# Kernel optimization log

Measured on AMD Instinct MI355X. Metric: run time of the kernel, lower is better.

## Reference

```python
import jax, jax.numpy as jnp
import numpy as np
import math

B, N, E, D = 8, 2048, 2048, 128
MAX_K = 8
HYPER_DIM = 128
LN_EPS = 1e-5


def _sinusoidal_pe(max_pos, dim):
    pe = np.zeros((max_pos, dim), dtype=np.float32)
    position = np.arange(max_pos, dtype=np.float32)[:, None]
    div_term = np.exp(np.arange(0, dim, 2, dtype=np.float32) * (-math.log(10000.0) / dim))
    pe[:, 0::2] = np.sin(position * div_term)
    pe[:, 1::2] = np.cos(position * div_term)
    return jnp.asarray(pe)


def setup_inputs() -> dict:
    key = jax.random.key(0)
    ks = jax.random.split(key, 24)
    s = 0.05
    inp = {
        'x_v': jax.random.normal(ks[0], (B, N, D), jnp.float32),
        'x_e': jax.random.normal(ks[1], (B, E, D), jnp.float32),
        'incidence': (jax.random.uniform(ks[2], (B, N, E), jnp.float32) < 0.01).astype(jnp.float32),
        'suffix_normalizer': jax.random.uniform(ks[3], (B, N), jnp.float32) * 20.0,
        'edge_orders': 1 + jax.random.randint(ks[4], (B, E), 0, MAX_K),
        'node_mask': jax.random.randint(ks[5], (B, N), 0, 2) > 0,
        'edge_mask': jax.random.randint(ks[6], (B, E), 0, 2) > 0,
        'pe1_table': _sinusoidal_pe(MAX_K + 1, D),
        'pe2_table': _sinusoidal_pe(2, D),
        'bias_b': jax.random.uniform(ks[7], (1, D), jnp.float32, -1, 1) / math.sqrt(D),
    }
    i = 8
    for m in ('mlp1', 'mlp2', 'mlp3'):
        inp[m + '_W1'] = jax.random.normal(ks[i], (D, HYPER_DIM), jnp.float32) * s; i += 1
        inp[m + '_b1'] = jnp.zeros((HYPER_DIM,), jnp.float32)
        inp[m + '_W2'] = jax.random.normal(ks[i], (HYPER_DIM, D), jnp.float32) * s; i += 1
        inp[m + '_b2'] = jnp.zeros((D,), jnp.float32)
    for n in ('norm1', 'norm2', 'norm3'):
        inp[n + '_g'] = jnp.ones((D,), jnp.float32)
        inp[n + '_b'] = jnp.zeros((D,), jnp.float32)
    return inp


def _ln(x, g, b):
    mu = jnp.mean(x, axis=-1, keepdims=True)
    var = jnp.mean(jnp.square(x - mu), axis=-1, keepdims=True)
    return (x - mu) * jax.lax.rsqrt(var + LN_EPS) * g + b


def _mlp(x, W1, b1, W2, b2):
    return jax.nn.relu(x @ W1 + b1) @ W2 + b2


def reference(x_v, x_e, incidence, suffix_normalizer, edge_orders, node_mask, edge_mask,
              pe1_table, pe2_table, bias_b,
              mlp1_W1, mlp1_b1, mlp1_W2, mlp1_b2,
              mlp2_W1, mlp2_b1, mlp2_W2, mlp2_b2,
              mlp3_W1, mlp3_b1, mlp3_W2, mlp3_b2,
              norm1_g, norm1_b, norm2_g, norm2_b, norm3_g, norm3_b):
    nm = node_mask[..., None]  # [B,N,1]
    em = edge_mask[..., None]  # [B,E,1]
    x_v = jnp.where(nm, x_v, 0.0)
    x_e = jnp.where(em, x_e, 0.0)
    pe1_k1 = pe1_table[1][None, None, :]          # [1,1,D]
    pe1_k = pe1_table[edge_orders]                # [B,E,D]
    x_v = x_v + _mlp(_ln(x_v, norm1_g, norm1_b) + pe1_k1, mlp1_W1, mlp1_b1, mlp1_W2, mlp1_b2)
    x_e = x_e + _mlp(_ln(x_e, norm1_g, norm1_b) + pe1_k, mlp1_W1, mlp1_b1, mlp1_W2, mlp1_b2)
    x_v = jnp.where(nm, x_v, 0.0)
    x_e = jnp.where(em, x_e, 0.0)
    agg = jnp.einsum('bne,bed->bnd', incidence, x_e)
    x1 = x_v + agg / (1.0 + suffix_normalizer[..., None])
    pe2_s1 = pe2_table[1][None, None, :]
    x1 = x1 + _mlp(_ln(x1, norm2_g, norm2_b) + pe2_s1, mlp2_W1, mlp2_b1, mlp2_W2, mlp2_b2)
    x = jnp.where(nm, x1, 0.0)
    x = x + _mlp(_ln(x, norm3_g, norm3_b), mlp3_W1, mlp3_b1, mlp3_W2, mlp3_b2)
    x = x + bias_b
    x = jnp.where(nm, x, 0.0)
    return x
```

## Files before the change

kernel.cpp:

```cpp
#include <hip/hip_runtime.h>
#include <stdint.h>

#define BB 8
#define NN 2048
#define EE 2048
#define DD 128
#define RBP 132
#define NTHREADS 256
#define WMAT_U32 8192
#define SCANB 2048
#define LCAP 64

typedef __attribute__((ext_vector_type(8))) short bf16x8;
typedef __attribute__((ext_vector_type(4))) float f32x4;

__device__ inline unsigned bf16rne(float f) {
    unsigned u = __float_as_uint(f);
    return (u + 0x7fffu + ((u >> 16) & 1u)) >> 16;
}
__device__ inline float bf16lo(unsigned u) { return __uint_as_float(u << 16); }
__device__ inline float bf16hi(unsigned u) { return __uint_as_float(u & 0xffff0000u); }

#define SWZ(b) ((b) ^ ((((b) >> 8) & 7) << 4))

struct __align__(16) SmemK1 {
    float rowbuf[32][RBP];
    unsigned h[32 * DD / 2];
    int rmask[32];
    int ords[32];
};

struct __align__(16) SmemK2 {
    float rowbuf[16][RBP];
    unsigned h[16 * DD / 2];
    int rmask[16];
};

__device__ inline void load_rows32(SmemK1& s, const float* __restrict__ src) {
    int t = threadIdx.x;
    for (int idx = t; idx < 32 * 32; idx += NTHREADS) {
        int r = idx >> 5, c4 = (idx & 31) * 4;
        float4 v = *(const float4*)&src[r * DD + c4];
        *(float4*)&s.rowbuf[r][c4] = v;
    }
    __syncthreads();
}

__device__ inline void ln32(SmemK1& s, const float* __restrict__ gw,
                            const float* __restrict__ bw,
                            const float* __restrict__ pe_base, bool per_row_pe) {
    int t = threadIdx.x;
    int gr = t >> 3, g = t & 7;
    int base = g * 16;
    float x[16];
    float4* xp = (float4*)x;
    xp[0] = *(const float4*)&s.rowbuf[gr][base + 0];
    xp[1] = *(const float4*)&s.rowbuf[gr][base + 4];
    xp[2] = *(const float4*)&s.rowbuf[gr][base + 8];
    xp[3] = *(const float4*)&s.rowbuf[gr][base + 12];
    float s1 = 0.f, s2 = 0.f;
    #pragma unroll
    for (int i = 0; i < 16; i++) { s1 += x[i]; s2 += x[i] * x[i]; }
    #pragma unroll
    for (int off = 1; off < 8; off <<= 1) {
        s1 += __shfl_xor(s1, off, 64);
        s2 += __shfl_xor(s2, off, 64);
    }
    float mu = s1 * (1.f / 128.f);
    float var = s2 * (1.f / 128.f) - mu * mu;
    float rstd = rsqrtf(var + 1e-5f);
    const float* pe = nullptr;
    if (pe_base) pe = per_row_pe ? (pe_base + (size_t)s.ords[gr] * DD) : pe_base;
    unsigned p[8];
    #pragma unroll
    for (int j = 0; j < 8; j++) {
        int k0 = base + 2 * j;
        float v0 = (x[2 * j] - mu) * rstd * gw[k0] + bw[k0];
        float v1 = (x[2 * j + 1] - mu) * rstd * gw[k0 + 1] + bw[k0 + 1];
        if (pe) { v0 += pe[k0]; v1 += pe[k0 + 1]; }
        p[j] = bf16rne(v0) | (bf16rne(v1) << 16);
    }
    char* hb = (char*)s.h;
    int byte0 = gr * 256 + g * 32;
    uint4 lo = make_uint4(p[0], p[1], p[2], p[3]);
    uint4 hi = make_uint4(p[4], p[5], p[6], p[7]);
    *(uint4*)(hb + SWZ(byte0)) = lo;
    *(uint4*)(hb + SWZ(byte0 + 16)) = hi;
    __syncthreads();
}

template <bool TO_H>
__device__ inline void mm32_f32w(SmemK1& s, const float* __restrict__ Wf,
                                 const float* __restrict__ bias) {
    int t = threadIdx.x;
    int w = t >> 6, l = t & 63;
    int lm = l & 15, lk = l >> 4;
    bf16x8 bfr[2][4];
    #pragma unroll
    for (int nbl = 0; nbl < 2; nbl++) {
        int n = w * 32 + nbl * 16 + lm;
        #pragma unroll
        for (int kb = 0; kb < 4; kb++) {
            int k0 = kb * 32 + lk * 8;
            unsigned pk[4];
            #pragma unroll
            for (int jp = 0; jp < 4; jp++) {
                float a = Wf[(size_t)(k0 + 2 * jp) * DD + n];
                float b = Wf[(size_t)(k0 + 2 * jp + 1) * DD + n];
                pk[jp] = bf16rne(a) | (bf16rne(b) << 16);
            }
            uint4 u = make_uint4(pk[0], pk[1], pk[2], pk[3]);
            bfr[nbl][kb] = *(bf16x8*)&u;
        }
    }
    const char* hb = (const char*)s.h;
    bf16x8 afr[2][4];
    #pragma unroll
    for (int mb = 0; mb < 2; mb++) {
        int row = mb * 16 + lm;
        #pragma unroll
        for (int kb = 0; kb < 4; kb++)
            afr[mb][kb] = *(const bf16x8*)(hb + SWZ(row * 256 + kb * 64 + lk * 16));
    }
    f32x4 acc[2][2];
    #pragma unroll
    for (int mb = 0; mb < 2; mb++)
        #pragma unroll
        for (int nbl = 0; nbl < 2; nbl++)
            acc[mb][nbl] = (f32x4){0.f, 0.f, 0.f, 0.f};
    #pragma unroll
    for (int kb = 0; kb < 4; kb++)
        #pragma unroll
        for (int mb = 0; mb < 2; mb++)
            #pragma unroll
            for (int nbl = 0; nbl < 2; nbl++)
                acc[mb][nbl] = __builtin_amdgcn_mfma_f32_16x16x32_bf16(
                    afr[mb][kb], bfr[nbl][kb], acc[mb][nbl], 0, 0, 0);
    float bcol0 = bias[w * 32 + lm];
    float bcol1 = bias[w * 32 + 16 + lm];
    __syncthreads();
    if (TO_H) {
        char* hw = (char*)s.h;
        #pragma unroll
        for (int mb = 0; mb < 2; mb++)
            #pragma unroll
            for (int nbl = 0; nbl < 2; nbl++) {
                int col = w * 32 + nbl * 16 + lm;
                float bc = nbl ? bcol1 : bcol0;
                #pragma unroll
                for (int j = 0; j < 4; j++) {
                    int row = mb * 16 + lk * 4 + j;
                    float v = fmaxf(acc[mb][nbl][j] + bc, 0.f);
                    *(unsigned short*)(hw + SWZ(row * 256 + col * 2)) =
                        (unsigned short)bf16rne(v);
                }
            }
    } else {
        #pragma unroll
        for (int mb = 0; mb < 2; mb++)
            #pragma unroll
            for (int nbl = 0; nbl < 2; nbl++) {
                int col = w * 32 + nbl * 16 + lm;
                float bc = nbl ? bcol1 : bcol0;
                #pragma unroll
                for (int j = 0; j < 4; j++) {
                    int row = mb * 16 + lk * 4 + j;
                    s.rowbuf[row][col] += acc[mb][nbl][j] + bc;
                }
            }
    }
    __syncthreads();
}

__device__ inline void scan2(const float* __restrict__ inc,
                             const int* __restrict__ nmask,
                             unsigned* __restrict__ lists, int* __restrict__ cnts,
                             int grow0) {
    int l = threadIdx.x & 63;
    unsigned long long lmlt = (1ull << l) - 1ull;
    int m0 = nmask[grow0];
    int m1 = nmask[grow0 + 1];
    const float4* ir0 = (const float4*)(inc + (size_t)grow0 * EE);
    const float4* ir1 = (const float4*)(inc + (size_t)(grow0 + 1) * EE);
    float4 v0[8], v1[8];
    if (m0) {
        #pragma unroll
        for (int i = 0; i < 8; i++) v0[i] = ir0[l + 64 * i];
    } else {
        #pragma unroll
        for (int i = 0; i < 8; i++) v0[i] = make_float4(0.f, 0.f, 0.f, 0.f);
    }
    if (m1) {
        #pragma unroll
        for (int i = 0; i < 8; i++) v1[i] = ir1[l + 64 * i];
    } else {
        #pragma unroll
        for (int i = 0; i < 8; i++) v1[i] = make_float4(0.f, 0.f, 0.f, 0.f);
    }
    unsigned* lp0 = lists + (size_t)grow0 * LCAP;
    unsigned* lp1 = lists + (size_t)(grow0 + 1) * LCAP;
    int t0 = 0, t1 = 0;
    #pragma unroll
    for (int i = 0; i < 8; i++) {
        #pragma unroll
        for (int c = 0; c < 4; c++) {
            float a = (c == 0) ? v0[i].x : (c == 1) ? v0[i].y : (c == 2) ? v0[i].z : v0[i].w;
            float b = (c == 0) ? v1[i].x : (c == 1) ? v1[i].y : (c == 2) ? v1[i].z : v1[i].w;
            bool na = (a != 0.f), nb = (b != 0.f);
            unsigned long long ka = __ballot(na);
            unsigned long long kb = __ballot(nb);
            unsigned e = (unsigned)((l + 64 * i) * 4 + c);
            if (na) {
                int p = t0 + __popcll(ka & lmlt);
                if (p < LCAP) lp0[p] = e;
            }
            if (nb) {
                int p = t1 + __popcll(kb & lmlt);
                if (p < LCAP) lp1[p] = e;
            }
            t0 += __popcll(ka);
            t1 += __popcll(kb);
        }
    }
    if (l == 0) {
        if (m0) cnts[grow0] = t0 > LCAP ? LCAP : t0;
        if (m1) cnts[grow0 + 1] = t1 > LCAP ? LCAP : t1;
    }
}

__device__ inline void ln16(SmemK2& s, const float* __restrict__ gw,
                            const float* __restrict__ bw,
                            const float* __restrict__ pe) {
    int t = threadIdx.x;
    int gr = t >> 4, g = t & 15;
    int base = g * 8;
    float x[8];
    float4* xp = (float4*)x;
    xp[0] = *(const float4*)&s.rowbuf[gr][base + 0];
    xp[1] = *(const float4*)&s.rowbuf[gr][base + 4];
    float s1 = 0.f, s2 = 0.f;
    #pragma unroll
    for (int i = 0; i < 8; i++) { s1 += x[i]; s2 += x[i] * x[i]; }
    #pragma unroll
    for (int off = 1; off < 16; off <<= 1) {
        s1 += __shfl_xor(s1, off, 64);
        s2 += __shfl_xor(s2, off, 64);
    }
    float mu = s1 * (1.f / 128.f);
    float var = s2 * (1.f / 128.f) - mu * mu;
    float rstd = rsqrtf(var + 1e-5f);
    unsigned p[4];
    #pragma unroll
    for (int j = 0; j < 4; j++) {
        int k0 = base + 2 * j;
        float v0 = (x[2 * j] - mu) * rstd * gw[k0] + bw[k0];
        float v1 = (x[2 * j + 1] - mu) * rstd * gw[k0 + 1] + bw[k0 + 1];
        if (pe) { v0 += pe[k0]; v1 += pe[k0 + 1]; }
        p[j] = bf16rne(v0) | (bf16rne(v1) << 16);
    }
    char* hb = (char*)s.h;
    uint4 q = make_uint4(p[0], p[1], p[2], p[3]);
    *(uint4*)(hb + SWZ(gr * 256 + g * 16)) = q;
    __syncthreads();
}

template <bool TO_H>
__device__ inline void mm16(SmemK2& s, const unsigned* __restrict__ WT,
                            const float* __restrict__ bias) {
    int t = threadIdx.x;
    int w = t >> 6, l = t & 63;
    int lm = l & 15, lk = l >> 4;
    bf16x8 bfr[2][4];
    const uint4* wt4 = (const uint4*)WT;
    #pragma unroll
    for (int nbl = 0; nbl < 2; nbl++) {
        int n = w * 32 + nbl * 16 + lm;
        #pragma unroll
        for (int kb = 0; kb < 4; kb++) {
            uint4 u = wt4[n * 16 + kb * 4 + lk];
            bfr[nbl][kb] = *(bf16x8*)&u;
        }
    }
    const char* hb = (const char*)s.h;
    bf16x8 afr[4];
    #pragma unroll
    for (int kb = 0; kb < 4; kb++)
        afr[kb] = *(const bf16x8*)(hb + SWZ(lm * 256 + kb * 64 + lk * 16));
    f32x4 acc[2];
    acc[0] = (f32x4){0.f, 0.f, 0.f, 0.f};
    acc[1] = (f32x4){0.f, 0.f, 0.f, 0.f};
    #pragma unroll
    for (int kb = 0; kb < 4; kb++)
        #pragma unroll
        for (int nbl = 0; nbl < 2; nbl++)
            acc[nbl] = __builtin_amdgcn_mfma_f32_16x16x32_bf16(
                afr[kb], bfr[nbl][kb], acc[nbl], 0, 0, 0);
    float bcol0 = bias[w * 32 + lm];
    float bcol1 = bias[w * 32 + 16 + lm];
    __syncthreads();
    if (TO_H) {
        char* hw = (char*)s.h;
        #pragma unroll
        for (int nbl = 0; nbl < 2; nbl++) {
            int col = w * 32 + nbl * 16 + lm;
            float bc = nbl ? bcol1 : bcol0;
            #pragma unroll
            for (int j = 0; j < 4; j++) {
                int row = lk * 4 + j;
                float v = fmaxf(acc[nbl][j] + bc, 0.f);
                *(unsigned short*)(hw + SWZ(row * 256 + col * 2)) =
                    (unsigned short)bf16rne(v);
            }
        }
    } else {
        #pragma unroll
        for (int nbl = 0; nbl < 2; nbl++) {
            int col = w * 32 + nbl * 16 + lm;
            float bc = nbl ? bcol1 : bcol0;
            #pragma unroll
            for (int j = 0; j < 4; j++) {
                int row = lk * 4 + j;
                s.rowbuf[row][col] += acc[nbl][j] + bc;
            }
        }
    }
    __syncthreads();
}

__device__ inline void gather16(SmemK2& s, int row0,
                                const unsigned* __restrict__ lists,
                                const int* __restrict__ cnts,
                                const unsigned* __restrict__ e2b,
                                const float* __restrict__ sn) {
    int t = threadIdx.x;
    int w = t >> 6, l = t & 63;
    int cnt[4]; unsigned pk[4]; float snv[4];
    #pragma unroll
    for (int i = 0; i < 4; i++) {
        int grow = row0 + w * 4 + i;
        pk[i] = lists[(size_t)grow * LCAP + l];
        snv[i] = sn[grow];
        cnt[i] = cnts[grow];
    }
    #pragma unroll
    for (int i = 0; i < 4; i++) {
        int r = w * 4 + i;
        if (s.rmask[r] == 0) continue;
        int cn = cnt[i]; if (cn > LCAP) cn = LCAP;
        float ax = 0.f, ay = 0.f;
        for (int j0 = 0; j0 < cn; j0 += 8) {
            int nn = cn - j0;
            unsigned uv[8];
            #pragma unroll
            for (int u = 0; u < 8; u++) {
                unsigned e = __shfl(pk[i], j0 + u, 64);
                uv[u] = (u < nn) ? e2b[(size_t)e * 64 + l] : 0u;
            }
            #pragma unroll
            for (int u = 0; u < 8; u++) { ax += bf16lo(uv[u]); ay += bf16hi(uv[u]); }
        }
        float inv = 1.f / (1.f + snv[i]);
        float2* rb = (float2*)&s.rowbuf[r][2 * l];
        float2 cur = *rb;
        cur.x += ax * inv;
        cur.y += ay * inv;
        *rb = cur;
    }
    __syncthreads();
}

__global__ __launch_bounds__(NTHREADS) void k1_kernel(
    const float* __restrict__ x_e, const int* __restrict__ emask,
    const int* __restrict__ nmask, const int* __restrict__ eord,
    const float* __restrict__ pe1, const float* __restrict__ inc,
    const float* __restrict__ n1g, const float* __restrict__ n1b,
    const float* __restrict__ W11, const float* __restrict__ b11,
    const float* __restrict__ W12, const float* __restrict__ b12,
    const float* __restrict__ W21, const float* __restrict__ W22,
    const float* __restrict__ W31, const float* __restrict__ W32,
    unsigned* __restrict__ WT, unsigned* __restrict__ e2pk,
    unsigned* __restrict__ lists, int* __restrict__ cnts) {
    __shared__ SmemK1 s;
    int bid = blockIdx.x;
    int t = threadIdx.x;
    if (bid < SCANB) {
        int gtid = bid * NTHREADS + t;
        if (gtid < 6 * WMAT_U32) {
            int mat = gtid >> 13;
            int idx = gtid & (WMAT_U32 - 1);
            int n = idx >> 6, j = idx & 63;
            const float* W = mat == 0 ? W11 : mat == 1 ? W12 : mat == 2 ? W21
                           : mat == 3 ? W22 : mat == 4 ? W31 : W32;
            float a = W[(2 * j) * DD + n];
            float b = W[(2 * j + 1) * DD + n];
            WT[gtid] = bf16rne(a) | (bf16rne(b) << 16);
        }
        int wid = bid * 4 + (t >> 6);
        scan2(inc, nmask, lists, cnts, wid * 2);
        return;
    }
    int lb = bid - SCANB;
    int bb = lb & 7;
    int e0 = (lb >> 3) * 32;
    int rowbase = bb * EE + e0;
    if (t < 32) {
        s.rmask[t] = emask[rowbase + t];
        int o = eord[rowbase + t];
        s.ords[t] = o < 0 ? 0 : (o > 8 ? 8 : o);
    }
    load_rows32(s, x_e + (size_t)rowbase * DD);
    ln32(s, n1g, n1b, pe1, true);
    mm32_f32w<true>(s, W11, b11);
    mm32_f32w<false>(s, W12, b12);
    unsigned* dst = e2pk + (size_t)rowbase * (DD / 2);
    for (int idx = t; idx < 32 * 16; idx += NTHREADS) {
        int r = idx >> 4, q = idx & 15;
        uint4 o = make_uint4(0u, 0u, 0u, 0u);
        if (s.rmask[r] != 0) {
            const float* rp = &s.rowbuf[r][q * 8];
            o.x = bf16rne(rp[0]) | (bf16rne(rp[1]) << 16);
            o.y = bf16rne(rp[2]) | (bf16rne(rp[3]) << 16);
            o.z = bf16rne(rp[4]) | (bf16rne(rp[5]) << 16);
            o.w = bf16rne(rp[6]) | (bf16rne(rp[7]) << 16);
        }
        *(uint4*)&dst[r * 64 + q * 4] = o;
    }
}

__global__ __launch_bounds__(NTHREADS) void k2_kernel(
    const float* __restrict__ x_v, const int* __restrict__ nmask,
    const float* __restrict__ sn,
    const float* __restrict__ pe1, const float* __restrict__ pe2,
    const float* __restrict__ biasb,
    const float* __restrict__ n1g, const float* __restrict__ n1b,
    const float* __restrict__ n2g, const float* __restrict__ n2b,
    const float* __restrict__ n3g, const float* __restrict__ n3b,
    const unsigned* __restrict__ WT,
    const float* __restrict__ b11, const float* __restrict__ b12,
    const float* __restrict__ b21, const float* __restrict__ b22,
    const float* __restrict__ b31, const float* __restrict__ b32,
    const unsigned* __restrict__ e2pk, const unsigned* __restrict__ lists,
    const int* __restrict__ cnts, float* __restrict__ out) {
    __shared__ SmemK2 s;
    int bid = blockIdx.x;
    int bb = bid & 7;
    int n0 = (bid >> 3) * 16;
    int row0 = bb * NN + n0;
    int t = threadIdx.x;
    if (t < 16) s.rmask[t] = nmask[row0 + t];
    for (int idx = t; idx < 16 * 32; idx += NTHREADS) {
        int r = idx >> 5, c4 = (idx & 31) * 4;
        float4 v = *(const float4*)&x_v[(size_t)(row0 + r) * DD + c4];
        *(float4*)&s.rowbuf[r][c4] = v;
    }
    __syncthreads();
    for (int idx = t; idx < 16 * 32; idx += NTHREADS) {
        int r = idx >> 5, c4 = (idx & 31) * 4;
        if (s.rmask[r] == 0) *(float4*)&s.rowbuf[r][c4] = make_float4(0.f, 0.f, 0.f, 0.f);
    }
    __syncthreads();
    ln16(s, n1g, n1b, pe1 + DD);
    mm16<true>(s, WT + 0 * WMAT_U32, b11);
    mm16<false>(s, WT + 1 * WMAT_U32, b12);
    gather16(s, row0, lists, cnts, e2pk + (size_t)bb * (EE * (DD / 2)), sn);
    ln16(s, n2g, n2b, pe2 + DD);
    mm16<true>(s, WT + 2 * WMAT_U32, b21);
    mm16<false>(s, WT + 3 * WMAT_U32, b22);
    ln16(s, n3g, n3b, nullptr);
    mm16<true>(s, WT + 4 * WMAT_U32, b31);
    mm16<false>(s, WT + 5 * WMAT_U32, b32);
    for (int idx = t; idx < 16 * 32; idx += NTHREADS) {
        int r = idx >> 5, c4 = (idx & 31) * 4;
        float4 v = make_float4(0.f, 0.f, 0.f, 0.f);
        if (s.rmask[r] != 0) {
            v = *(const float4*)&s.rowbuf[r][c4];
            float4 bbv = *(const float4*)&biasb[c4];
            v.x += bbv.x; v.y += bbv.y; v.z += bbv.z; v.w += bbv.w;
        }
        *(float4*)&out[(size_t)(row0 + r) * DD + c4] = v;
    }
}

extern "C" void kernel_launch(void* const* d_in, const int* in_sizes, int n_in,
                              void* d_out, int out_size, void* d_ws, size_t ws_size,
                              hipStream_t stream) {
    const float* x_v   = (const float*)d_in[0];
    const float* x_e   = (const float*)d_in[1];
    const float* inc   = (const float*)d_in[2];
    const float* sn    = (const float*)d_in[3];
    const int*   eord  = (const int*)d_in[4];
    const int*   nmask = (const int*)d_in[5];
    const int*   emask = (const int*)d_in[6];
    const float* pe1   = (const float*)d_in[7];
    const float* pe2   = (const float*)d_in[8];
    const float* biasb = (const float*)d_in[9];
    const float* W11   = (const float*)d_in[10];
    const float* b11   = (const float*)d_in[11];
    const float* W12   = (const float*)d_in[12];
    const float* b12   = (const float*)d_in[13];
    const float* W21   = (const float*)d_in[14];
    const float* b21   = (const float*)d_in[15];
    const float* W22   = (const float*)d_in[16];
    const float* b22   = (const float*)d_in[17];
    const float* W31   = (const float*)d_in[18];
    const float* b31   = (const float*)d_in[19];
    const float* W32   = (const float*)d_in[20];
    const float* b32   = (const float*)d_in[21];
    const float* n1g   = (const float*)d_in[22];
    const float* n1b   = (const float*)d_in[23];
    const float* n2g   = (const float*)d_in[24];
    const float* n2b   = (const float*)d_in[25];
    const float* n3g   = (const float*)d_in[26];
    const float* n3b   = (const float*)d_in[27];

    unsigned* e2pk  = (unsigned*)d_ws;
    unsigned* WT    = e2pk + (size_t)BB * EE * (DD / 2);
    unsigned* lists = WT + 6 * WMAT_U32;
    int*      cnts  = (int*)(lists + (size_t)BB * NN * LCAP);
    float*    out   = (float*)d_out;

    dim3 blk(NTHREADS);
    k1_kernel<<<dim3(SCANB + BB * EE / 32), blk, 0, stream>>>(
        x_e, emask, nmask, eord, pe1, inc,
        n1g, n1b, W11, b11, W12, b12, W21, W22, W31, W32,
        WT, e2pk, lists, cnts);
    k2_kernel<<<dim3(BB * NN / 16), blk, 0, stream>>>(
        x_v, nmask, sn, pe1, pe2, biasb,
        n1g, n1b, n2g, n2b, n3g, n3b,
        WT, b11, b12, b21, b22, b31, b32,
        e2pk, lists, cnts, out);
}
```

Measured before the change: 66.80 us.

## Move node-side MLP1 into first kernel and split incidence scan one row per warp

The node-side LN+MLP1 moves from the second kernel into the first kernel's MLP blocks, which now handle both edge and node rows. The intermediate node state goes to the output buffer, and the second kernel reads it back and overwrites it in place. The incidence scan now gives one row per warp across twice as many blocks, and the weight bf16 conversion moves to the MLP blocks. The aim is to shorten the serial chain in the second kernel and balance work between launches, at the cost of an extra global write and read of the node activations.

```diff
diff --git a/kernel.cpp b/kernel.cpp
--- a/kernel.cpp
+++ b/kernel.cpp
@@ -8,7 +8,8 @@
 #define RBP 132
 #define NTHREADS 256
 #define WMAT_U32 8192
-#define SCANB 2048
+#define SCANB 4096
+#define MLPB 1024
 #define LCAP 64
 
 typedef __attribute__((ext_vector_type(8))) short bf16x8;
@@ -42,6 +43,11 @@
         int r = idx >> 5, c4 = (idx & 31) * 4;
         float4 v = *(const float4*)&src[r * DD + c4];
         *(float4*)&s.rowbuf[r][c4] = v;
+    }
+    __syncthreads();
+    for (int idx = t; idx < 32 * 32; idx += NTHREADS) {
+        int r = idx >> 5, c4 = (idx & 31) * 4;
+        if (s.rmask[r] == 0) *(float4*)&s.rowbuf[r][c4] = make_float4(0.f, 0.f, 0.f, 0.f);
     }
     __syncthreads();
 }
@@ -172,60 +178,34 @@
     __syncthreads();
 }
 
-__device__ inline void scan2(const float* __restrict__ inc,
+__device__ inline void scan1(const float* __restrict__ inc,
                              const int* __restrict__ nmask,
                              unsigned* __restrict__ lists, int* __restrict__ cnts,
-                             int grow0) {
+                             int grow) {
     int l = threadIdx.x & 63;
+    if (nmask[grow] == 0) return;
     unsigned long long lmlt = (1ull << l) - 1ull;
-    int m0 = nmask[grow0];
-    int m1 = nmask[grow0 + 1];
-    const float4* ir0 = (const float4*)(inc + (size_t)grow0 * EE);
-    const float4* ir1 = (const float4*)(inc + (size_t)(grow0 + 1) * EE);
-    float4 v0[8], v1[8];
-    if (m0) {
-        #pragma unroll
-        for (int i = 0; i < 8; i++) v0[i] = ir0[l + 64 * i];
-    } else {
-        #pragma unroll
-        for (int i = 0; i < 8; i++) v0[i] = make_float4(0.f, 0.f, 0.f, 0.f);
-    }
-    if (m1) {
-        #pragma unroll
-        for (int i = 0; i < 8; i++) v1[i] = ir1[l + 64 * i];
-    } else {
-        #pragma unroll
-        for (int i = 0; i < 8; i++) v1[i] = make_float4(0.f, 0.f, 0.f, 0.f);
-    }
-    unsigned* lp0 = lists + (size_t)grow0 * LCAP;
-    unsigned* lp1 = lists + (size_t)(grow0 + 1) * LCAP;
-    int t0 = 0, t1 = 0;
+    const float4* ir = (const float4*)(inc + (size_t)grow * EE);
+    float4 v[8];
+    #pragma unroll
+    for (int i = 0; i < 8; i++) v[i] = ir[l + 64 * i];
+    unsigned* lp = lists + (size_t)grow * LCAP;
+    int total = 0;
     #pragma unroll
     for (int i = 0; i < 8; i++) {
         #pragma unroll
         for (int c = 0; c < 4; c++) {
-            float a = (c == 0) ? v0[i].x : (c == 1) ? v0[i].y : (c == 2) ? v0[i].z : v0[i].w;
-            float b = (c == 0) ? v1[i].x : (c == 1) ? v1[i].y : (c == 2) ? v1[i].z : v1[i].w;
-            bool na = (a != 0.f), nb = (b != 0.f);
-            unsigned long long ka = __ballot(na);
-            unsigned long long kb = __ballot(nb);
-            unsigned e = (unsigned)((l + 64 * i) * 4 + c);
-            if (na) {
-                int p = t0 + __popcll(ka & lmlt);
-                if (p < LCAP) lp0[p] = e;
-            }
-            if (nb) {
-                int p = t1 + __popcll(kb & lmlt);
-                if (p < LCAP) lp1[p] = e;
-            }
-            t0 += __popcll(ka);
-            t1 += __popcll(kb);
-        }
-    }
-    if (l == 0) {
-        if (m0) cnts[grow0] = t0 > LCAP ? LCAP : t0;
-        if (m1) cnts[grow0 + 1] = t1 > LCAP ? LCAP : t1;
-    }
+            float a = (c == 0) ? v[i].x : (c == 1) ? v[i].y : (c == 2) ? v[i].z : v[i].w;
+            bool nz = (a != 0.f);
+            unsigned long long msk = __ballot(nz);
+            if (nz) {
+                int p = total + __popcll(msk & lmlt);
+                if (p < LCAP) lp[p] = (unsigned)((l + 64 * i) * 4 + c);
+            }
+            total += __popcll(msk);
+        }
+    }
+    if (l == 0) cnts[grow] = total > LCAP ? LCAP : total;
 }
 
 __device__ inline void ln16(SmemK2& s, const float* __restrict__ gw,
@@ -370,73 +350,86 @@
 }
 
 __global__ __launch_bounds__(NTHREADS) void k1_kernel(
-    const float* __restrict__ x_e, const int* __restrict__ emask,
-    const int* __restrict__ nmask, const int* __restrict__ eord,
-    const float* __restrict__ pe1, const float* __restrict__ inc,
+    const float* __restrict__ x_e, const float* __restrict__ x_v,
+    const int* __restrict__ emask, const int* __restrict__ nmask,
+    const int* __restrict__ eord, const float* __restrict__ pe1,
+    const float* __restrict__ inc,
     const float* __restrict__ n1g, const float* __restrict__ n1b,
     const float* __restrict__ W11, const float* __restrict__ b11,
     const float* __restrict__ W12, const float* __restrict__ b12,
     const float* __restrict__ W21, const float* __restrict__ W22,
     const float* __restrict__ W31, const float* __restrict__ W32,
     unsigned* __restrict__ WT, unsigned* __restrict__ e2pk,
+    float* __restrict__ v2out,
     unsigned* __restrict__ lists, int* __restrict__ cnts) {
+    int bid = blockIdx.x;
+    int t = threadIdx.x;
+    if (bid < SCANB) {
+        scan1(inc, nmask, lists, cnts, bid * 4 + (t >> 6));
+        return;
+    }
     __shared__ SmemK1 s;
-    int bid = blockIdx.x;
-    int t = threadIdx.x;
-    if (bid < SCANB) {
-        int gtid = bid * NTHREADS + t;
-        if (gtid < 6 * WMAT_U32) {
-            int mat = gtid >> 13;
-            int idx = gtid & (WMAT_U32 - 1);
-            int n = idx >> 6, j = idx & 63;
-            const float* W = mat == 0 ? W11 : mat == 1 ? W12 : mat == 2 ? W21
-                           : mat == 3 ? W22 : mat == 4 ? W31 : W32;
-            float a = W[(2 * j) * DD + n];
-            float b = W[(2 * j + 1) * DD + n];
-            WT[gtid] = bf16rne(a) | (bf16rne(b) << 16);
-        }
-        int wid = bid * 4 + (t >> 6);
-        scan2(inc, nmask, lists, cnts, wid * 2);
-        return;
-    }
     int lb = bid - SCANB;
-    int bb = lb & 7;
-    int e0 = (lb >> 3) * 32;
-    int rowbase = bb * EE + e0;
+    int gtid = lb * NTHREADS + t;
+    if (gtid < 6 * WMAT_U32) {
+        int mat = gtid >> 13;
+        int idx = gtid & (WMAT_U32 - 1);
+        int n = idx >> 6, j = idx & 63;
+        const float* W = mat == 0 ? W11 : mat == 1 ? W12 : mat == 2 ? W21
+                       : mat == 3 ? W22 : mat == 4 ? W31 : W32;
+        float a = W[(2 * j) * DD + n];
+        float b = W[(2 * j + 1) * DD + n];
+        WT[gtid] = bf16rne(a) | (bf16rne(b) << 16);
+    }
+    bool isEdge = lb < (BB * EE / 32);
+    int mb = isEdge ? lb : lb - (BB * EE / 32);
+    int bb = mb & 7;
+    int r0 = (mb >> 3) * 32;
+    int rowbase = bb * EE + r0;
+    const int* mask = isEdge ? emask : nmask;
     if (t < 32) {
-        s.rmask[t] = emask[rowbase + t];
-        int o = eord[rowbase + t];
-        s.ords[t] = o < 0 ? 0 : (o > 8 ? 8 : o);
-    }
-    load_rows32(s, x_e + (size_t)rowbase * DD);
-    ln32(s, n1g, n1b, pe1, true);
+        s.rmask[t] = mask[rowbase + t];
+        if (isEdge) {
+            int o = eord[rowbase + t];
+            s.ords[t] = o < 0 ? 0 : (o > 8 ? 8 : o);
+        }
+    }
+    __syncthreads();
+    load_rows32(s, (isEdge ? x_e : x_v) + (size_t)rowbase * DD);
+    ln32(s, n1g, n1b, isEdge ? pe1 : (pe1 + DD), isEdge);
     mm32_f32w<true>(s, W11, b11);
     mm32_f32w<false>(s, W12, b12);
-    unsigned* dst = e2pk + (size_t)rowbase * (DD / 2);
-    for (int idx = t; idx < 32 * 16; idx += NTHREADS) {
-        int r = idx >> 4, q = idx & 15;
-        uint4 o = make_uint4(0u, 0u, 0u, 0u);
-        if (s.rmask[r] != 0) {
-            const float* rp = &s.rowbuf[r][q * 8];
-            o.x = bf16rne(rp[0]) | (bf16rne(rp[1]) << 16);
-            o.y = bf16rne(rp[2]) | (bf16rne(rp[3]) << 16);
-            o.z = bf16rne(rp[4]) | (bf16rne(rp[5]) << 16);
-            o.w = bf16rne(rp[6]) | (bf16rne(rp[7]) << 16);
-        }
-        *(uint4*)&dst[r * 64 + q * 4] = o;
+    if (isEdge) {
+        unsigned* dst = e2pk + (size_t)rowbase * (DD / 2);
+        for (int idx = t; idx < 32 * 16; idx += NTHREADS) {
+            int r = idx >> 4, q = idx & 15;
+            uint4 o = make_uint4(0u, 0u, 0u, 0u);
+            if (s.rmask[r] != 0) {
+                const float* rp = &s.rowbuf[r][q * 8];
+                o.x = bf16rne(rp[0]) | (bf16rne(rp[1]) << 16);
+                o.y = bf16rne(rp[2]) | (bf16rne(rp[3]) << 16);
+                o.z = bf16rne(rp[4]) | (bf16rne(rp[5]) << 16);
+                o.w = bf16rne(rp[6]) | (bf16rne(rp[7]) << 16);
+            }
+            *(uint4*)&dst[r * 64 + q * 4] = o;
+        }
+    } else {
+        for (int idx = t; idx < 32 * 32; idx += NTHREADS) {
+            int r = idx >> 5, c4 = (idx & 31) * 4;
+            float4 v = make_float4(0.f, 0.f, 0.f, 0.f);
+            if (s.rmask[r] != 0) v = *(const float4*)&s.rowbuf[r][c4];
+            *(float4*)&v2out[(size_t)(rowbase + r) * DD + c4] = v;
+        }
     }
 }
 
 __global__ __launch_bounds__(NTHREADS) void k2_kernel(
-    const float* __restrict__ x_v, const int* __restrict__ nmask,
+    const float* __restrict__ v2, const int* __restrict__ nmask,
     const float* __restrict__ sn,
-    const float* __restrict__ pe1, const float* __restrict__ pe2,
-    const float* __restrict__ biasb,
-    const float* __restrict__ n1g, const float* __restrict__ n1b,
+    const float* __restrict__ pe2, const float* __restrict__ biasb,
     const float* __restrict__ n2g, const float* __restrict__ n2b,
     const float* __restrict__ n3g, const float* __restrict__ n3b,
     const unsigned* __restrict__ WT,
-    const float* __restrict__ b11, const float* __restrict__ b12,
     const float* __restrict__ b21, const float* __restrict__ b22,
     const float* __restrict__ b31, const float* __restrict__ b32,
     const unsigned* __restrict__ e2pk, const unsigned* __restrict__ lists,
@@ -450,18 +443,10 @@
     if (t < 16) s.rmask[t] = nmask[row0 + t];
     for (int idx = t; idx < 16 * 32; idx += NTHREADS) {
         int r = idx >> 5, c4 = (idx & 31) * 4;
-        float4 v = *(const float4*)&x_v[(size_t)(row0 + r) * DD + c4];
+        float4 v = *(const float4*)&v2[(size_t)(row0 + r) * DD + c4];
         *(float4*)&s.rowbuf[r][c4] = v;
     }
     __syncthreads();
-    for (int idx = t; idx < 16 * 32; idx += NTHREADS) {
-        int r = idx >> 5, c4 = (idx & 31) * 4;
-        if (s.rmask[r] == 0) *(float4*)&s.rowbuf[r][c4] = make_float4(0.f, 0.f, 0.f, 0.f);
-    }
-    __syncthreads();
-    ln16(s, n1g, n1b, pe1 + DD);
-    mm16<true>(s, WT + 0 * WMAT_U32, b11);
-    mm16<false>(s, WT + 1 * WMAT_U32, b12);
     gather16(s, row0, lists, cnts, e2pk + (size_t)bb * (EE * (DD / 2)), sn);
     ln16(s, n2g, n2b, pe2 + DD);
     mm16<true>(s, WT + 2 * WMAT_U32, b21);
@@ -520,13 +505,13 @@
     float*    out   = (float*)d_out;
 
     dim3 blk(NTHREADS);
-    k1_kernel<<<dim3(SCANB + BB * EE / 32), blk, 0, stream>>>(
-        x_e, emask, nmask, eord, pe1, inc,
+    k1_kernel<<<dim3(SCANB + MLPB), blk, 0, stream>>>(
+        x_e, x_v, emask, nmask, eord, pe1, inc,
         n1g, n1b, W11, b11, W12, b12, W21, W22, W31, W32,
-        WT, e2pk, lists, cnts);
+        WT, e2pk, out, lists, cnts);
     k2_kernel<<<dim3(BB * NN / 16), blk, 0, stream>>>(
-        x_v, nmask, sn, pe1, pe2, biasb,
-        n1g, n1b, n2g, n2b, n3g, n3b,
-        WT, b11, b12, b21, b22, b31, b32,
+        out, nmask, sn, pe2, biasb,
+        n2g, n2b, n3g, n3b,
+        WT, b21, b22, b31, b32,
         e2pk, lists, cnts, out);
 }
```

New measurement: 62.92 us. 1.06x faster.
